# Kernel tuning notes

Hardware: AMD Instinct MI355X
Metric: run time of the kernel (lower is better)

Reference implementation:

```python
import jax, jax.numpy as jnp
import numpy as np

EPS = 1e-5  # batchnorm epsilon

def _bin11(t):
    # binarize to {-1, +1}; sign with 0 -> +1
    return jnp.where(t >= 0, jnp.ones((), t.dtype), -jnp.ones((), t.dtype))

def setup_inputs() -> dict:
    key = jax.random.key(0)
    k1, k2, k3, k4, k5 = jax.random.split(key, 5)
    B = 8192
    sizes = [4096, 4096, 4096, 1024]
    x = jax.random.uniform(k1, (B, sizes[0]), dtype=jnp.float32)
    W0 = jax.random.normal(k2, (sizes[0], sizes[1]), dtype=jnp.float32)
    W1 = jax.random.normal(k3, (sizes[1], sizes[2]), dtype=jnp.float32)
    W2 = jax.random.normal(k4, (sizes[2], sizes[3]), dtype=jnp.float32)
    gamma = jax.random.uniform(k5, (3,), dtype=jnp.float32)  # uniform_ init in source
    beta = jnp.zeros((3,), dtype=jnp.float32)
    return {"x": x, "W0": W0, "W1": W1, "W2": W2, "gamma": gamma, "beta": beta}

def reference(x, W0, W1, W2, gamma, beta):
    Ws = [W0, W1, W2]
    L = len(Ws)
    # a[-1] = x - 0.5; ab = binarize11(a[-1])
    ab = _bin11(x - 0.5)
    a = None
    for k in range(L):
        Wb = _bin11(Ws[k])
        s = jnp.matmul(ab, Wb)  # [B, out_k]
        # training-mode batchnorm with per-output batch stats, scalar gamma/beta per layer
        mu = jnp.mean(s, axis=0)
        var = jnp.var(s, axis=0)
        a = (s - mu) * jax.lax.rsqrt(var + EPS) * gamma[k] + beta[k]
        if k < L - 1:
            ab = _bin11(a)
    # torch.nn.Softmax(dim=0): softmax across the batch dimension, as in source
    return jax.nn.softmax(a, axis=0)
```

## Files before the change

### kernel.cpp

```cpp
#include <hip/hip_runtime.h>
#include <stdint.h>

typedef unsigned long long u64;
typedef int v4i  __attribute__((ext_vector_type(4)));
typedef int v16i __attribute__((ext_vector_type(16)));

#define B_ROWS 8192
#define K_BITS 4096
#define KW 64
#define GBM 256
#define GBN 256

__global__ void init_stats(int* sum0, u64* sq0, int* sum1, u64* sq1,
                           int* sum2, u64* sq2, int* smax, int* smin, float* esum,
                           int* rp0, int* rp1, int* rp2, int* cp0, int* cp1, int* cp2) {
  int i = blockIdx.x * 256 + threadIdx.x;
  if (i < 8192) { rp0[i] = 0; rp1[i] = 0; rp2[i] = 0; }
  if (i < 4096) { sum0[i] = 0; sq0[i] = 0; sum1[i] = 0; sq1[i] = 0; cp0[i] = 0; cp1[i] = 0; }
  if (i < 1024) {
    sum2[i] = 0; sq2[i] = 0; cp2[i] = 0;
    smax[i] = (int)0x80000000; smin[i] = 0x7fffffff;
    esum[i] = 0.0f;
  }
}

__global__ __launch_bounds__(256)
void pack_x(const float* __restrict__ x, u64* __restrict__ bits,
            int* __restrict__ rp) {
  const int row = blockIdx.x;
  const int t = threadIdx.x;
  const float4* p = (const float4*)(x + (size_t)row * K_BITS + 16 * t);
  unsigned m = 0;
  #pragma unroll
  for (int q = 0; q < 4; q++) {
    float4 v = p[q];
    m |= (unsigned)(v.x >= 0.5f) << (4 * q + 0);
    m |= (unsigned)(v.y >= 0.5f) << (4 * q + 1);
    m |= (unsigned)(v.z >= 0.5f) << (4 * q + 2);
    m |= (unsigned)(v.w >= 0.5f) << (4 * q + 3);
  }
  ((unsigned short*)bits)[(size_t)row * 256 + t] = (unsigned short)m;
  int pc = __popc(m);
  #pragma unroll
  for (int off = 32; off; off >>= 1) pc += __shfl_down(pc, off);
  __shared__ int acc4[4];
  if ((t & 63) == 0) acc4[t >> 6] = pc;
  __syncthreads();
  if (t == 0) rp[row] = acc4[0] + acc4[1] + acc4[2] + acc4[3];
}

__global__ void pack_w(const float* __restrict__ W, u64* __restrict__ Wb,
                       int N, int nlog2, int* __restrict__ cp) {
  int t = blockIdx.x * 256 + threadIdx.x;
  int n = t & (N - 1);
  int w = t >> nlog2;
  const float* p = W + (size_t)(w * 64) * N + n;
  u64 m = 0;
  #pragma unroll 8
  for (int b = 0; b < 64; b++)
    m |= (u64)(p[(size_t)b * N] >= 0.0f) << b;
  Wb[(size_t)n * KW + w] = m;
  atomicAdd(&cp[n], (int)__popcll(m));
}

__device__ __forceinline__ v4i unpack16(unsigned word, int shbase) {
  v4i r;
  #pragma unroll
  for (int q = 0; q < 4; q++) {
    unsigned nib = (word >> (shbase + 4 * q)) & 15u;
    r[q] = (int)(__umul24(nib, 0x00204081u) & 0x01010101u);
  }
  return r;
}

__global__ __launch_bounds__(512, 2)
void gemm_mfma(const u64* __restrict__ Ab, const u64* __restrict__ Wb,
               short* __restrict__ S, int N,
               const int* __restrict__ rp, const int* __restrict__ cp,
               int* __restrict__ colsum, u64* __restrict__ colsq,
               int* __restrict__ colmax, int* __restrict__ colmin, int dominmax) {
  __shared__ alignas(16) u64 AsB[256][2];
  __shared__ alignas(16) u64 BsB[256][2];
  __shared__ int rp_s[256];
  __shared__ int redS[4][256];
  __shared__ int redQ[4][256];

  const int tid  = threadIdx.x;
  const int lane = tid & 63;
  const int wid  = tid >> 6;
  const int wm   = wid >> 2;
  const int wn   = wid & 3;
  const int half = lane >> 5;
  const int l31  = lane & 31;
  const int row0 = blockIdx.y * GBM, col0 = blockIdx.x * GBN;

  if (tid < 256) rp_s[tid] = rp[row0 + tid];

  v16i acc[4][2];
  #pragma unroll
  for (int mt = 0; mt < 4; mt++)
    #pragma unroll
    for (int nt = 0; nt < 2; nt++)
      #pragma unroll
      for (int e = 0; e < 16; e++) acc[mt][nt][e] = 0;

  const int srow = tid >> 1, sw = tid & 1;
  const u64* aptr = Ab + (size_t)(row0 + srow) * KW + sw;
  const u64* bptr = Wb + (size_t)(col0 + srow) * KW + sw;

  u64 areg = aptr[0], breg = bptr[0];

  for (int ch = 0; ch < 32; ch++) {
    AsB[srow][sw] = areg;
    BsB[srow][sw] = breg;
    __syncthreads();
    if (ch < 31) { areg = aptr[2 * (ch + 1)]; breg = bptr[2 * (ch + 1)]; }
    uint4 abits[4]; uint4 bbits[2];
    #pragma unroll
    for (int mt = 0; mt < 4; mt++)
      abits[mt] = *(const uint4*)&AsB[wm * 128 + mt * 32 + l31][0];
    #pragma unroll
    for (int nt = 0; nt < 2; nt++)
      bbits[nt] = *(const uint4*)&BsB[wn * 64 + nt * 32 + l31][0];
    __syncthreads();
    #pragma unroll
    for (int ks = 0; ks < 4; ks++) {
      v4i afrag[4], bfrag[2];
      #pragma unroll
      for (int mt = 0; mt < 4; mt++) {
        unsigned wa = (ks == 0) ? abits[mt].x : (ks == 1) ? abits[mt].y
                    : (ks == 2) ? abits[mt].z : abits[mt].w;
        afrag[mt] = unpack16(wa, half * 16);
      }
      #pragma unroll
      for (int nt = 0; nt < 2; nt++) {
        unsigned wb = (ks == 0) ? bbits[nt].x : (ks == 1) ? bbits[nt].y
                    : (ks == 2) ? bbits[nt].z : bbits[nt].w;
        bfrag[nt] = unpack16(wb, half * 16);
      }
      #pragma unroll
      for (int mt = 0; mt < 4; mt++)
        #pragma unroll
        for (int nt = 0; nt < 2; nt++)
          acc[mt][nt] = __builtin_amdgcn_mfma_i32_32x32x32_i8(
              afrag[mt], bfrag[nt], acc[mt][nt], 0, 0, 0);
    }
  }

  int cpv[2];
  #pragma unroll
  for (int nt = 0; nt < 2; nt++) cpv[nt] = cp[col0 + wn * 64 + nt * 32 + l31];

  int ps[2], pq[2], mx[2], mn[2];
  #pragma unroll
  for (int nt = 0; nt < 2; nt++) { ps[nt] = 0; pq[nt] = 0; mx[nt] = -100000; mn[nt] = 100000; }

  #pragma unroll
  for (int mt = 0; mt < 4; mt++) {
    #pragma unroll
    for (int reg = 0; reg < 16; reg++) {
      int rloc = wm * 128 + mt * 32 + (reg & 3) + 8 * (reg >> 2) + 4 * half;
      int rpv  = rp_s[rloc];
      size_t rowoff = (size_t)(row0 + rloc) * N + col0;
      #pragma unroll
      for (int nt = 0; nt < 2; nt++) {
        int s = 4 * acc[mt][nt][reg] - 2 * rpv - 2 * cpv[nt] + K_BITS;
        S[rowoff + wn * 64 + nt * 32 + l31] = (short)s;
        ps[nt] += s;
        pq[nt] += s * s;
        mx[nt] = (s > mx[nt]) ? s : mx[nt];
        mn[nt] = (s < mn[nt]) ? s : mn[nt];
      }
    }
  }

  const int contrib = wm * 2 + half;
  #pragma unroll
  for (int nt = 0; nt < 2; nt++) {
    redS[contrib][wn * 64 + nt * 32 + l31] = ps[nt];
    redQ[contrib][wn * 64 + nt * 32 + l31] = pq[nt];
  }
  __syncthreads();
  if (tid < 256) {
    int ssum = 0; long long sq = 0;
    #pragma unroll
    for (int t = 0; t < 4; t++) { ssum += redS[t][tid]; sq += (long long)redQ[t][tid]; }
    atomicAdd(&colsum[col0 + tid], ssum);
    atomicAdd(&colsq[col0 + tid], (u64)sq);
  }
  if (dominmax) {
    __syncthreads();
    #pragma unroll
    for (int nt = 0; nt < 2; nt++) {
      redS[contrib][wn * 64 + nt * 32 + l31] = mx[nt];
      redQ[contrib][wn * 64 + nt * 32 + l31] = mn[nt];
    }
    __syncthreads();
    if (tid < 256) {
      int m1 = -100000, m2 = 100000;
      #pragma unroll
      for (int t = 0; t < 4; t++) {
        m1 = (redS[t][tid] > m1) ? redS[t][tid] : m1;
        m2 = (redQ[t][tid] < m2) ? redQ[t][tid] : m2;
      }
      atomicMax(&colmax[col0 + tid], m1);
      atomicMin(&colmin[col0 + tid], m2);
    }
  }
}

__global__ void stats01(const int* __restrict__ colsum, const u64* __restrict__ colsq,
                        const float* __restrict__ gamma, int layer, float* __restrict__ c) {
  int n = blockIdx.x * 256 + threadIdx.x;
  double mu  = (double)colsum[n] / 8192.0;
  double var = (double)colsq[n] / 8192.0 - mu * mu;
  c[n] = (float)((double)gamma[layer] / sqrt(var + 1e-5));
}

__global__ void binarize_pack(const short* __restrict__ S, const int* __restrict__ colsum,
                              const float* __restrict__ c, const float* __restrict__ beta,
                              int layer, u64* __restrict__ bits, int* __restrict__ rpn) {
  int gwave = (blockIdx.x * 256 + threadIdx.x) >> 6;
  int lane = threadIdx.x & 63;
  int idx0 = (gwave << 7) + lane;
  int idx1 = idx0 + 64;
  int n0 = idx0 & (K_BITS - 1);
  int n1 = idx1 & (K_BITS - 1);
  float bv = beta[layer];
  int t0 = (int)S[idx0] * 8192 - colsum[n0];
  int t1 = (int)S[idx1] * 8192 - colsum[n1];
  float a0 = (float)t0 * c[n0] * (1.0f / 8192.0f) + bv;
  float a1 = (float)t1 * c[n1] * (1.0f / 8192.0f) + bv;
  u64 m0 = __ballot(a0 >= 0.0f);
  u64 m1 = __ballot(a1 >= 0.0f);
  if (lane == 0) {
    bits[(gwave << 1) + 0] = m0;
    bits[(gwave << 1) + 1] = m1;
    atomicAdd(&rpn[idx0 >> 12], (int)(__popcll(m0) + __popcll(m1)));
  }
}

__global__ void final_stats(const int* __restrict__ colsum, const u64* __restrict__ colsq,
                            const int* __restrict__ colmax, const int* __restrict__ colmin,
                            const float* __restrict__ gamma,
                            float* __restrict__ c, int* __restrict__ sref) {
  int n = blockIdx.x * 256 + threadIdx.x;
  double mu  = (double)colsum[n] / 8192.0;
  double var = (double)colsq[n] / 8192.0 - mu * mu;
  float cv = (float)((double)gamma[2] / sqrt(var + 1e-5));
  c[n] = cv;
  sref[n] = (cv >= 0.0f) ? colmax[n] : colmin[n];
}

__global__ void softmax_p1(const short* __restrict__ S2, const int* __restrict__ sref,
                           const float* __restrict__ c, float* __restrict__ out,
                           float* __restrict__ esum) {
  int n  = blockIdx.x * 256 + threadIdx.x;
  int r0 = blockIdx.y * 128;
  float cs = c[n]; int sr = sref[n];
  float acc = 0.0f;
  for (int r = 0; r < 128; r++) {
    size_t idx = (size_t)(r0 + r) * 1024 + n;
    float e = __expf((float)((int)S2[idx] - sr) * cs);
    out[idx] = e;
    acc += e;
  }
  atomicAdd(&esum[n], acc);
}

__global__ void softmax_p2(float* __restrict__ out, const float* __restrict__ esum) {
  int idx = blockIdx.x * 256 + threadIdx.x;
  out[idx] /= esum[idx & 1023];
}

extern "C" void kernel_launch(void* const* d_in, const int* in_sizes, int n_in,
                              void* d_out, int out_size, void* d_ws, size_t ws_size,
                              hipStream_t stream) {
  const float* x     = (const float*)d_in[0];
  const float* W0    = (const float*)d_in[1];
  const float* W1    = (const float*)d_in[2];
  const float* W2    = (const float*)d_in[3];
  const float* gamma = (const float*)d_in[4];
  const float* beta  = (const float*)d_in[5];
  float* out = (float*)d_out;

  char* ws = (char*)d_ws;
  u64*   bitsA = (u64*)(ws + 0);
  u64*   bitsB = (u64*)(ws + (4ull  << 20));
  u64*   Wb0   = (u64*)(ws + (8ull  << 20));
  u64*   Wb1   = (u64*)(ws + (10ull << 20));
  u64*   Wb2   = (u64*)(ws + (12ull << 20));
  short* S     = (short*)(ws + (16ull << 20));
  char*  st    = ws + (80ull << 20);
  int*   sum0 = (int*)(st);
  u64*   sq0  = (u64*)(st + 16 * 1024);
  int*   sum1 = (int*)(st + 48 * 1024);
  u64*   sq1  = (u64*)(st + 64 * 1024);
  int*   sum2 = (int*)(st + 96 * 1024);
  u64*   sq2  = (u64*)(st + 100 * 1024);
  int*   smax = (int*)(st + 108 * 1024);
  int*   smin = (int*)(st + 112 * 1024);
  float* c0   = (float*)(st + 116 * 1024);
  float* c1   = (float*)(st + 132 * 1024);
  float* c2   = (float*)(st + 148 * 1024);
  int*   sref = (int*)(st + 152 * 1024);
  float* esum = (float*)(st + 156 * 1024);
  int*   rp0  = (int*)(st + 160 * 1024);
  int*   rp1  = (int*)(st + 192 * 1024);
  int*   rp2  = (int*)(st + 224 * 1024);
  int*   cp0  = (int*)(st + 256 * 1024);
  int*   cp1  = (int*)(st + 272 * 1024);
  int*   cp2  = (int*)(st + 288 * 1024);

  init_stats<<<32, 256, 0, stream>>>(sum0, sq0, sum1, sq1, sum2, sq2, smax, smin, esum,
                                     rp0, rp1, rp2, cp0, cp1, cp2);
  pack_x<<<B_ROWS, 256, 0, stream>>>(x, bitsA, rp0);
  pack_w<<<(4096 * 64) / 256, 256, 0, stream>>>(W0, Wb0, 4096, 12, cp0);
  pack_w<<<(4096 * 64) / 256, 256, 0, stream>>>(W1, Wb1, 4096, 12, cp1);
  pack_w<<<(1024 * 64) / 256, 256, 0, stream>>>(W2, Wb2, 1024, 10, cp2);

  gemm_mfma<<<dim3(16, 32), 512, 0, stream>>>(bitsA, Wb0, S, 4096, rp0, cp0,
                                              sum0, sq0, nullptr, nullptr, 0);
  stats01<<<16, 256, 0, stream>>>(sum0, sq0, gamma, 0, c0);
  binarize_pack<<<(B_ROWS * 4096) / 512, 256, 0, stream>>>(S, sum0, c0, beta, 0, bitsB, rp1);

  gemm_mfma<<<dim3(16, 32), 512, 0, stream>>>(bitsB, Wb1, S, 4096, rp1, cp1,
                                              sum1, sq1, nullptr, nullptr, 0);
  stats01<<<16, 256, 0, stream>>>(sum1, sq1, gamma, 1, c1);
  binarize_pack<<<(B_ROWS * 4096) / 512, 256, 0, stream>>>(S, sum1, c1, beta, 1, bitsA, rp2);

  gemm_mfma<<<dim3(4, 32), 512, 0, stream>>>(bitsA, Wb2, S, 1024, rp2, cp2,
                                             sum2, sq2, smax, smin, 1);
  final_stats<<<4, 256, 0, stream>>>(sum2, sq2, smax, smin, gamma, c2, sref);
  softmax_p1<<<dim3(4, 64), 256, 0, stream>>>(S, sref, c2, out, esum);
  softmax_p2<<<(B_ROWS * 1024) / 256, 256, 0, stream>>>(out, esum);
}
```

Measured before the change: 772.2 us.

## Double-buffer bit tiles in LDS and interleave MFMA with unpack ALU

Converts the single-buffered LDS staging of packed A/W bit chunks into a ping-pong buffer, so each chunk iteration needs only one barrier instead of two. The next chunk is written into the alternate buffer while the current one is read. It also adds sched_group_barrier hints to interleave each MFMA with about nine VALU ops from the bit unpacking, aiming to hide unpack latency behind matrix instructions. The cost is double the LDS for the bit tiles and a deeper global prefetch. Scheduling hints can also constrain the compiler and raise register pressure.

```diff
diff --git a/kernel.cpp b/kernel.cpp
--- a/kernel.cpp
+++ b/kernel.cpp
@@ -79,8 +79,8 @@
                const int* __restrict__ rp, const int* __restrict__ cp,
                int* __restrict__ colsum, u64* __restrict__ colsq,
                int* __restrict__ colmax, int* __restrict__ colmin, int dominmax) {
-  __shared__ alignas(16) u64 AsB[256][2];
-  __shared__ alignas(16) u64 BsB[256][2];
+  __shared__ alignas(16) u64 AsB[2][256][2];
+  __shared__ alignas(16) u64 BsB[2][256][2];
   __shared__ int rp_s[256];
   __shared__ int redS[4][256];
   __shared__ int redQ[4][256];
@@ -108,21 +108,32 @@
   const u64* aptr = Ab + (size_t)(row0 + srow) * KW + sw;
   const u64* bptr = Wb + (size_t)(col0 + srow) * KW + sw;
 
-  u64 areg = aptr[0], breg = bptr[0];
-
+  {
+    u64 a0 = aptr[0], b0 = bptr[0];
+    AsB[0][srow][sw] = a0; BsB[0][srow][sw] = b0;
+  }
+  u64 areg = aptr[2], breg = bptr[2];
+
+  #pragma unroll 1
   for (int ch = 0; ch < 32; ch++) {
-    AsB[srow][sw] = areg;
-    BsB[srow][sw] = breg;
     __syncthreads();
-    if (ch < 31) { areg = aptr[2 * (ch + 1)]; breg = bptr[2 * (ch + 1)]; }
-    uint4 abits[4]; uint4 bbits[2];
+    const int cur = ch & 1;
+    if (ch < 31) {
+      AsB[cur ^ 1][srow][sw] = areg;
+      BsB[cur ^ 1][srow][sw] = breg;
+    }
+    if (ch < 30) {
+      areg = aptr[2 * (ch + 2)];
+      breg = bptr[2 * (ch + 2)];
+    }
+    uint4 abits[4], bbits[2];
     #pragma unroll
     for (int mt = 0; mt < 4; mt++)
-      abits[mt] = *(const uint4*)&AsB[wm * 128 + mt * 32 + l31][0];
+      abits[mt] = *(const uint4*)&AsB[cur][wm * 128 + mt * 32 + l31][0];
     #pragma unroll
     for (int nt = 0; nt < 2; nt++)
-      bbits[nt] = *(const uint4*)&BsB[wn * 64 + nt * 32 + l31][0];
-    __syncthreads();
+      bbits[nt] = *(const uint4*)&BsB[cur][wn * 64 + nt * 32 + l31][0];
+
     #pragma unroll
     for (int ks = 0; ks < 4; ks++) {
       v4i afrag[4], bfrag[2];
@@ -144,6 +155,11 @@
         for (int nt = 0; nt < 2; nt++)
           acc[mt][nt] = __builtin_amdgcn_mfma_i32_32x32x32_i8(
               afrag[mt], bfrag[nt], acc[mt][nt], 0, 0, 0);
+      #pragma unroll
+      for (int q = 0; q < 8; q++) {
+        __builtin_amdgcn_sched_group_barrier(0x008, 1, 0);
+        __builtin_amdgcn_sched_group_barrier(0x002, 9, 0);
+      }
     }
   }
 
```

After: 814.1 us. 1.05x slower.
